# Optimization experiments

Measured on AMD Instinct MI355X. Metric: run time of the kernel, lower is better.

## Reference

```python
import jax, jax.numpy as jnp
import numpy as np

B, NN, F, H = 8, 1024, 256, 8
D = F // H
SCALE = D ** -0.5


def setup_inputs() -> dict:
    key = jax.random.key(0)
    ks = jax.random.split(key, 12)
    s = 0.02
    inp = {
        'ndata': jax.random.normal(ks[0], (B, NN, F), jnp.float32),
        'N': NN,
        'attn_bias': jax.random.normal(ks[1], (B, NN, NN, H), jnp.float32),
        'attn_mask': jax.random.randint(ks[2], (B, NN, NN), 0, 2).astype(bool),
        'Wq': jax.random.normal(ks[3], (F, F), jnp.float32) * s,
        'bq': jnp.zeros((F,), jnp.float32),
        'Wk': jax.random.normal(ks[4], (F, F), jnp.float32) * s,
        'bk': jnp.zeros((F,), jnp.float32),
        'Wv': jax.random.normal(ks[5], (F, F), jnp.float32) * s,
        'bv': jnp.zeros((F,), jnp.float32),
        'Wo': jax.random.normal(ks[6], (F, F), jnp.float32) * s,
        'bo': jnp.zeros((F,), jnp.float32),
    }
    return inp


def reference(ndata, N, attn_bias, attn_mask, Wq, bq, Wk, bk, Wv, bv, Wo, bo):
    b, n, f = ndata.shape
    # QKV projections (torch nn.Linear: x @ W.T + b), split heads
    q = (ndata @ Wq.T + bq).reshape(b, n, H, D) * SCALE
    k = (ndata @ Wk.T + bk).reshape(b, n, H, D)
    v = (ndata @ Wv.T + bv).reshape(b, n, H, D)
    # scores: (b, q, k, h) matching torch layout after its transposes
    scores = jnp.einsum('bqhd,bkhd->bqkh', q, k)
    scores = scores + attn_bias  # additive bias
    # original code force-unmasks column 0 so every row has a valid entry
    mask = attn_mask.at[:, :, 0].set(False)
    scores = jnp.where(mask[..., None], -jnp.inf, scores)
    attn = jax.nn.softmax(scores, axis=2)  # softmax over keys
    out = jnp.einsum('bqkh,bkhd->bqhd', attn, v).reshape(b, n, f)
    return out @ Wo.T + bo
```

## Files before the change

### kernel.cpp

```cpp
#include <hip/hip_runtime.h>
#include <hip/hip_bf16.h>

typedef __attribute__((ext_vector_type(8))) short short8;
typedef __attribute__((ext_vector_type(4))) float f32x4;

#define MFMA16(a,b,c) __builtin_amdgcn_mfma_f32_16x16x32_bf16((a),(b),(c),0,0,0)

static __device__ __forceinline__ unsigned int f2bf(float f){
    unsigned int u = __float_as_uint(f);
    u += 0x7FFFu + ((u >> 16) & 1u);
    return u >> 16;
}

static __device__ __forceinline__ short8 pack8(float4 a, float4 b){
    short8 r;
    r[0]=(short)f2bf(a.x); r[1]=(short)f2bf(a.y);
    r[2]=(short)f2bf(a.z); r[3]=(short)f2bf(a.w);
    r[4]=(short)f2bf(b.x); r[5]=(short)f2bf(b.y);
    r[6]=(short)f2bf(b.z); r[7]=(short)f2bf(b.w);
    return r;
}

__global__ void detect_mask_k(const int* __restrict__ m, int* __restrict__ flag){
    __shared__ int any_hi;
    if (threadIdx.x == 0) any_hi = 0;
    __syncthreads();
    int acc = 0;
    #pragma unroll
    for (int it = 0; it < 16; ++it)
        acc |= m[it*256 + threadIdx.x];
    if (acc & 0xFFFFFF00) atomicOr(&any_hi, 1);
    __syncthreads();
    if (threadIdx.x == 0) *flag = any_hi;
}

__global__ __launch_bounds__(256) void mask_prep_k(
    const unsigned int* __restrict__ m, const int* __restrict__ flag,
    unsigned int* __restrict__ bmout)
{
    const int tid  = threadIdx.x;
    const int lane = tid & 63;
    const unsigned int gbase = blockIdx.x*256u + tid;
    if (*flag == 0){
        for (int it = 0; it < 32; ++it){
            unsigned int idx = it*262144u + gbase;
            unsigned int v = m[idx];
            unsigned long long bal = __ballot(v != 0u);
            if (lane == 0)
                *(unsigned long long*)(bmout + (idx >> 5)) = bal;
        }
    } else {
        for (int it = 0; it < 8; ++it){
            unsigned int idx = it*262144u + gbase;
            unsigned int v = m[idx];
            unsigned int nib = (v | (v>>7) | (v>>14) | (v>>21)) & 0xFu;
            unsigned int x = nib << ((lane & 7)*4);
            x |= (unsigned int)__shfl_xor((int)x, 1);
            x |= (unsigned int)__shfl_xor((int)x, 2);
            x |= (unsigned int)__shfl_xor((int)x, 4);
            if ((lane & 7) == 0)
                bmout[idx >> 3] = x;
        }
    }
}

__global__ __launch_bounds__(256) void qkv_proj_k(
    const float* __restrict__ nd,
    const float* __restrict__ Wqp, const float* __restrict__ bqp,
    const float* __restrict__ Wkp, const float* __restrict__ bkp,
    const float* __restrict__ Wvp, const float* __restrict__ bvp,
    unsigned short* __restrict__ qout, unsigned short* __restrict__ kout,
    unsigned short* __restrict__ vtout)
{
    __shared__ __align__(16) unsigned short xl[64*264];
    const int tid  = threadIdx.x;
    const int bi   = blockIdx.x;
    const int kind = bi >> 7;
    const int R0   = (bi & 127) * 64;
    const int b    = R0 >> 10;
    const int n0   = R0 & 1023;

    #pragma unroll
    for (int it = 0; it < 16; ++it){
        int f4 = it*256 + tid;
        int r = f4 >> 6, c4 = f4 & 63;
        float4 v = *(const float4*)(nd + (size_t)(R0+r)*256 + c4*4);
        unsigned int lo = f2bf(v.x) | (f2bf(v.y) << 16);
        unsigned int hi = f2bf(v.z) | (f2bf(v.w) << 16);
        *(uint2*)&xl[r*264 + c4*4] = make_uint2(lo, hi);
    }
    __syncthreads();

    const int lane = tid & 63;
    const int w  = tid >> 6;
    const int ln = lane & 15;
    const int g  = lane >> 4;
    const int ow = w * 64;

    f32x4 acc[4][4];
    #pragma unroll
    for (int a=0;a<4;++a){
        #pragma unroll
        for (int c=0;c<4;++c) acc[a][c] = (f32x4){0.f,0.f,0.f,0.f};
    }

    if (kind < 2){
        const float* W  = kind ? Wkp : Wqp;
        const float* bb = kind ? bkp : bqp;
        unsigned short* op = kind ? kout : qout;
        const float scl = kind ? 1.0f : 0.17677669529663687f;
        for (int kk = 0; kk < 8; ++kk){
            short8 wf[4], xf[4];
            #pragma unroll
            for (int ot=0; ot<4; ++ot){
                const float* wp = W + (size_t)(ow + ot*16 + ln)*256 + kk*32 + g*8;
                wf[ot] = pack8(*(const float4*)wp, *(const float4*)(wp+4));
            }
            #pragma unroll
            for (int nt=0; nt<4; ++nt)
                xf[nt] = *(const short8*)&xl[(nt*16+ln)*264 + kk*32 + g*8];
            #pragma unroll
            for (int ot=0; ot<4; ++ot){
                #pragma unroll
                for (int nt=0; nt<4; ++nt)
                    acc[ot][nt] = MFMA16(wf[ot], xf[nt], acc[ot][nt]);
            }
        }
        #pragma unroll
        for (int ot=0; ot<4; ++ot){
            int o0 = ow + ot*16 + g*4;
            int h = o0 >> 5, d0 = o0 & 31;
            float4 b4 = *(const float4*)(bb + o0);
            #pragma unroll
            for (int nt=0; nt<4; ++nt){
                int n = n0 + nt*16 + ln;
                unsigned int lo = f2bf((acc[ot][nt][0]+b4.x)*scl) | (f2bf((acc[ot][nt][1]+b4.y)*scl)<<16);
                unsigned int hi = f2bf((acc[ot][nt][2]+b4.z)*scl) | (f2bf((acc[ot][nt][3]+b4.w)*scl)<<16);
                *(uint2*)(op + ((size_t)(b*8+h)*1024 + n)*32 + d0) = make_uint2(lo,hi);
            }
        }
    } else {
        for (int kk = 0; kk < 8; ++kk){
            short8 wf[4], xf[4];
            #pragma unroll
            for (int ot=0; ot<4; ++ot){
                const float* wp = Wvp + (size_t)(ow + ot*16 + ln)*256 + kk*32 + g*8;
                wf[ot] = pack8(*(const float4*)wp, *(const float4*)(wp+4));
            }
            #pragma unroll
            for (int nt=0; nt<4; ++nt)
                xf[nt] = *(const short8*)&xl[(nt*16+ln)*264 + kk*32 + g*8];
            #pragma unroll
            for (int nt=0; nt<4; ++nt){
                #pragma unroll
                for (int ot=0; ot<4; ++ot)
                    acc[nt][ot] = MFMA16(xf[nt], wf[ot], acc[nt][ot]);
            }
        }
        #pragma unroll
        for (int nt=0; nt<4; ++nt){
            int nb = n0 + nt*16 + g*4;
            #pragma unroll
            for (int ot=0; ot<4; ++ot){
                int o = ow + ot*16 + ln;
                int h = o >> 5, d = o & 31;
                float bvv = bvp[o];
                unsigned int lo = f2bf(acc[nt][ot][0]+bvv) | (f2bf(acc[nt][ot][1]+bvv)<<16);
                unsigned int hi = f2bf(acc[nt][ot][2]+bvv) | (f2bf(acc[nt][ot][3]+bvv)<<16);
                *(uint2*)(vtout + ((size_t)(b*8+h)*32 + d)*1024 + nb) = make_uint2(lo,hi);
            }
        }
    }
}

__global__ __launch_bounds__(512, 4) void attn_k(
    const unsigned short* __restrict__ qbuf, const unsigned short* __restrict__ kbuf,
    const unsigned short* __restrict__ vtbuf, const float* __restrict__ bias,
    const unsigned int* __restrict__ bm, unsigned short* __restrict__ ab)
{
    __shared__ float bs[4096];
    const int tid  = threadIdx.x;
    const int bi   = blockIdx.x;
    const int b    = bi >> 6;
    const int q0   = (bi & 63) * 16;
    const int lane = tid & 63;
    const int w    = tid >> 6;
    const int ln   = lane & 15;
    const int g    = lane >> 4;

    const short8 qf = *(const short8*)(qbuf + ((size_t)(b*8+w)*1024 + q0 + ln)*32 + g*8);

    const int h2s  = lane & 1;
    const int keys = lane >> 1;
    const int ts   = keys >> 4;
    const int rs   = keys & 3;
    const int gs   = (keys >> 2) & 3;
    const int base0 = (128*ts + 32*rs + 16*h2s + gs) * 16;
    const int xrs   = (8*ts + 2*rs + h2s) & 15;
    const int qxa   = (2*w)     ^ xrs;
    const int qxb   = (2*w + 1) ^ xrs;

    const float* bp0 = bias + ((size_t)(b*1024 + q0 + 2*w)*1024)*8 + lane*4;
    const unsigned short* kp = kbuf  + ((size_t)(b*8+w)*1024 + ln)*32 + g*8;
    const unsigned short* vp = vtbuf + ((size_t)(b*8+w)*32   + ln)*1024 + g*8;
    const unsigned int*  bmp = bm + (size_t)(b*1024 + q0 + ln)*32;

    f32x4 acc0 = (f32x4){0.f,0.f,0.f,0.f};
    f32x4 acc1 = (f32x4){0.f,0.f,0.f,0.f};
    float m_ = -1e30f, l_ = 0.f;
    const f32x4 z4 = {0.f,0.f,0.f,0.f};

    float4 ba  = *(const float4*)(bp0);
    float4 bb2 = *(const float4*)(bp0 + 8192);
    short8 kn0 = *(const short8*)(kp);
    short8 kn1 = *(const short8*)(kp + 512);
    short8 vn0 = *(const short8*)(vp);
    short8 vn1 = *(const short8*)(vp + 16*1024);
    unsigned int bmn = bmp[0] & ~1u;

    for (int c = 0; c < 32; ++c){
        bs[base0       + qxa] = ba.x;  bs[base0 +  64 + qxa] = ba.y;
        bs[base0 + 128 + qxa] = ba.z;  bs[base0 + 192 + qxa] = ba.w;
        bs[base0       + qxb] = bb2.x; bs[base0 +  64 + qxb] = bb2.y;
        bs[base0 + 128 + qxb] = bb2.z; bs[base0 + 192 + qxb] = bb2.w;

        short8 kc0 = kn0, kc1 = kn1, vc0 = vn0, vc1 = vn1;
        unsigned int bmc = bmn;

        if (c < 31){
            int c1 = c + 1;
            ba  = *(const float4*)(bp0 + c1*256);
            bb2 = *(const float4*)(bp0 + c1*256 + 8192);
            kn0 = *(const short8*)(kp + c1*1024);
            kn1 = *(const short8*)(kp + c1*1024 + 512);
            vn0 = *(const short8*)(vp + c1*32);
            vn1 = *(const short8*)(vp + c1*32 + 16*1024);
            bmn = bmp[c1];
        }
        __syncthreads();

        f32x4 s0 = MFMA16(kc0, qf, z4);
        f32x4 s1 = MFMA16(kc1, qf, z4);

        float pv[8];
        float mx = -1e30f;
        #pragma unroll
        for (int t=0; t<2; ++t){
            #pragma unroll
            for (int r=0; r<4; ++r){
                int keyl = t*16 + g*4 + r;
                int bidx = (t*128 + r*32 + w*4 + g)*16 + (ln ^ ((t*8 + r*2 + (w>>2)) & 15));
                float sv = (t ? s1[r] : s0[r]) + bs[bidx];
                sv = ((bmc >> keyl) & 1u) ? -1e30f : sv;
                pv[t*4+r] = sv;
                mx = fmaxf(mx, sv);
            }
        }
        mx = fmaxf(mx, __shfl_xor(mx, 16));
        mx = fmaxf(mx, __shfl_xor(mx, 32));
        float mn = fmaxf(m_, mx);
        float alpha = __expf(m_ - mn);
        m_ = mn;
        float ps = 0.f;
        #pragma unroll
        for (int i=0;i<8;++i){ pv[i] = __expf(pv[i]-mn); ps += pv[i]; }
        ps += __shfl_xor(ps, 16);
        ps += __shfl_xor(ps, 32);
        l_ = l_*alpha + ps;
        #pragma unroll
        for (int r=0;r<4;++r){ acc0[r]*=alpha; acc1[r]*=alpha; }

        unsigned int A01 = f2bf(pv[0]) | (f2bf(pv[1])<<16);
        unsigned int A23 = f2bf(pv[2]) | (f2bf(pv[3])<<16);
        unsigned int B01 = f2bf(pv[4]) | (f2bf(pv[5])<<16);
        unsigned int B23 = f2bf(pv[6]) | (f2bf(pv[7])<<16);
        int s0l = (2*(g&1))*16 + ln;
        int s1l = s0l + 16;
        unsigned int a01  = (unsigned int)__shfl((int)A01, s0l);
        unsigned int a23  = (unsigned int)__shfl((int)A23, s0l);
        unsigned int b01  = (unsigned int)__shfl((int)B01, s0l);
        unsigned int b23  = (unsigned int)__shfl((int)B23, s0l);
        unsigned int a01b = (unsigned int)__shfl((int)A01, s1l);
        unsigned int a23b = (unsigned int)__shfl((int)A23, s1l);
        unsigned int b01b = (unsigned int)__shfl((int)B01, s1l);
        unsigned int b23b = (unsigned int)__shfl((int)B23, s1l);
        bool hi = (g >= 2);
        int4 pw = make_int4((int)(hi ? b01  : a01 ), (int)(hi ? b23  : a23 ),
                            (int)(hi ? b01b : a01b), (int)(hi ? b23b : a23b));
        short8 pf = *(short8*)&pw;

        acc0 = MFMA16(vc0, pf, acc0);
        acc1 = MFMA16(vc1, pf, acc1);
        __syncthreads();
    }

    float inv = 1.0f / l_;
    {
        int n = q0 + ln;
        unsigned int lo0 = f2bf(acc0[0]*inv) | (f2bf(acc0[1]*inv)<<16);
        unsigned int hi0 = f2bf(acc0[2]*inv) | (f2bf(acc0[3]*inv)<<16);
        *(uint2*)(ab + ((size_t)(b*1024 + n))*256 + w*32 + g*4) = make_uint2(lo0,hi0);
        unsigned int lo1 = f2bf(acc1[0]*inv) | (f2bf(acc1[1]*inv)<<16);
        unsigned int hi1 = f2bf(acc1[2]*inv) | (f2bf(acc1[3]*inv)<<16);
        *(uint2*)(ab + ((size_t)(b*1024 + n))*256 + w*32 + 16 + g*4) = make_uint2(lo1,hi1);
    }
}

__global__ __launch_bounds__(256) void oproj_k(
    const unsigned short* __restrict__ ab, const float* __restrict__ Wop,
    const float* __restrict__ bop, float* __restrict__ out)
{
    __shared__ __align__(16) unsigned short al[32*264];
    const int tid = threadIdx.x;
    const int R0 = blockIdx.x * 32;
    #pragma unroll
    for (int it=0; it<4; ++it){
        int f8 = it*256 + tid;
        int r = f8 >> 5, c8 = f8 & 31;
        *(short8*)&al[r*264 + c8*8] = *(const short8*)(ab + (size_t)(R0+r)*256 + c8*8);
    }
    __syncthreads();
    const int lane = tid & 63;
    const int w = tid >> 6, ln = lane & 15, g = lane >> 4;
    const int ow = w*64;
    f32x4 acc[4][2];
    #pragma unroll
    for (int a=0;a<4;++a){ acc[a][0]=(f32x4){0.f,0.f,0.f,0.f}; acc[a][1]=(f32x4){0.f,0.f,0.f,0.f}; }
    for (int kk=0;kk<8;++kk){
        short8 wf[4], xf[2];
        #pragma unroll
        for (int ot=0;ot<4;++ot){
            const float* wp = Wop + (size_t)(ow+ot*16+ln)*256 + kk*32 + g*8;
            wf[ot] = pack8(*(const float4*)wp, *(const float4*)(wp+4));
        }
        #pragma unroll
        for (int nt=0;nt<2;++nt)
            xf[nt] = *(const short8*)&al[(nt*16+ln)*264 + kk*32 + g*8];
        #pragma unroll
        for (int ot=0;ot<4;++ot){
            #pragma unroll
            for (int nt=0;nt<2;++nt)
                acc[ot][nt] = MFMA16(wf[ot], xf[nt], acc[ot][nt]);
        }
    }
    #pragma unroll
    for (int ot=0;ot<4;++ot){
        int o0 = ow + ot*16 + g*4;
        float4 b4 = *(const float4*)(bop + o0);
        #pragma unroll
        for (int nt=0;nt<2;++nt){
            int n = R0 + nt*16 + ln;
            float4 res;
            res.x = acc[ot][nt][0] + b4.x;
            res.y = acc[ot][nt][1] + b4.y;
            res.z = acc[ot][nt][2] + b4.z;
            res.w = acc[ot][nt][3] + b4.w;
            *(float4*)(out + (size_t)n*256 + o0) = res;
        }
    }
}

extern "C" void kernel_launch(void* const* d_in, const int* in_sizes, int n_in,
                              void* d_out, int out_size, void* d_ws, size_t ws_size,
                              hipStream_t stream)
{
    (void)in_sizes; (void)n_in; (void)out_size; (void)ws_size;
    const float* nd   = (const float*)d_in[0];
    const float* bias = (const float*)d_in[2];
    const int* mask   = (const int*)d_in[3];
    const float* Wq = (const float*)d_in[4];
    const float* bq = (const float*)d_in[5];
    const float* Wk = (const float*)d_in[6];
    const float* bk = (const float*)d_in[7];
    const float* Wv = (const float*)d_in[8];
    const float* bv = (const float*)d_in[9];
    const float* Wo = (const float*)d_in[10];
    const float* bo = (const float*)d_in[11];
    float* out = (float*)d_out;

    const size_t ELEMS = (size_t)8*8*1024*32;
    unsigned short* qb  = (unsigned short*)d_ws;
    unsigned short* kb  = qb  + ELEMS;
    unsigned short* vtb = kb  + ELEMS;
    unsigned short* ab  = vtb + ELEMS;
    unsigned int* bmw   = (unsigned int*)(ab + ELEMS);
    int* mflag          = (int*)(bmw + 262144);

    detect_mask_k<<<1, 256, 0, stream>>>(mask, mflag);
    mask_prep_k<<<1024, 256, 0, stream>>>((const unsigned int*)mask, mflag, bmw);
    qkv_proj_k<<<384, 256, 0, stream>>>(nd, Wq, bq, Wk, bk, Wv, bv, qb, kb, vtb);
    attn_k<<<512, 512, 0, stream>>>(qb, kb, vtb, bias, bmw, ab);
    oproj_k<<<256, 256, 0, stream>>>(ab, Wo, bo, out);
}
```

Baseline: 146.9 us.

## Drop online softmax max tracking, split heads across blocks, fuse mask detection

Removes the running-max and rescaling from the attention softmax. It exponentiates biased scores directly and sums them per lane, reducing across lanes once at the end. Keys are permuted so P fragments line up with the MFMA layout without cross-lane shuffles, and each block now handles 4 heads instead of 8, doubling the grid. The loop is unrolled 2x with double-buffered K/V loads, and the separate mask-detection kernel is folded into mask_prep, with the format check now made per block. Skipping the max subtraction risks overflow when scores or biases are large.

New measurement: 170.3 us. 1.16x slower.

```diff
diff --git a/kernel.cpp b/kernel.cpp
--- a/kernel.cpp
+++ b/kernel.cpp
@@ -21,27 +21,26 @@
     return r;
 }
 
-__global__ void detect_mask_k(const int* __restrict__ m, int* __restrict__ flag){
+__global__ __launch_bounds__(256) void mask_prep_k(
+    const unsigned int* __restrict__ m, unsigned int* __restrict__ bmout)
+{
     __shared__ int any_hi;
-    if (threadIdx.x == 0) any_hi = 0;
-    __syncthreads();
-    int acc = 0;
-    #pragma unroll
-    for (int it = 0; it < 16; ++it)
-        acc |= m[it*256 + threadIdx.x];
-    if (acc & 0xFFFFFF00) atomicOr(&any_hi, 1);
-    __syncthreads();
-    if (threadIdx.x == 0) *flag = any_hi;
-}
-
-__global__ __launch_bounds__(256) void mask_prep_k(
-    const unsigned int* __restrict__ m, const int* __restrict__ flag,
-    unsigned int* __restrict__ bmout)
-{
     const int tid  = threadIdx.x;
     const int lane = tid & 63;
     const unsigned int gbase = blockIdx.x*256u + tid;
-    if (*flag == 0){
+    if (tid == 0) any_hi = 0;
+
+    unsigned int wv[8]; unsigned int acc = 0;
+    #pragma unroll
+    for (int it = 0; it < 8; ++it){
+        wv[it] = m[it*262144u + gbase];
+        acc |= wv[it];
+    }
+    __syncthreads();
+    if (acc & 0xFFFFFF00u) atomicOr(&any_hi, 1);
+    __syncthreads();
+
+    if (any_hi == 0){
         for (int it = 0; it < 32; ++it){
             unsigned int idx = it*262144u + gbase;
             unsigned int v = m[idx];
@@ -50,9 +49,10 @@
                 *(unsigned long long*)(bmout + (idx >> 5)) = bal;
         }
     } else {
+        #pragma unroll
         for (int it = 0; it < 8; ++it){
             unsigned int idx = it*262144u + gbase;
-            unsigned int v = m[idx];
+            unsigned int v = wv[it];
             unsigned int nib = (v | (v>>7) | (v>>14) | (v>>21)) & 0xFu;
             unsigned int x = nib << ((lane & 7)*4);
             x |= (unsigned int)__shfl_xor((int)x, 1);
@@ -173,137 +173,125 @@
     }
 }
 
-__global__ __launch_bounds__(512, 4) void attn_k(
+__global__ __launch_bounds__(256, 4) void attn_k(
     const unsigned short* __restrict__ qbuf, const unsigned short* __restrict__ kbuf,
     const unsigned short* __restrict__ vtbuf, const float* __restrict__ bias,
     const unsigned int* __restrict__ bm, unsigned short* __restrict__ ab)
 {
-    __shared__ float bs[4096];
+    __shared__ float bs[2048];
     const int tid  = threadIdx.x;
     const int bi   = blockIdx.x;
-    const int b    = bi >> 6;
-    const int q0   = (bi & 63) * 16;
+    const int hh   = bi & 1;
+    const int qt   = (bi >> 1) & 63;
+    const int b    = bi >> 7;
+    const int q0   = qt * 16;
     const int lane = tid & 63;
     const int w    = tid >> 6;
     const int ln   = lane & 15;
     const int g    = lane >> 4;
-
-    const short8 qf = *(const short8*)(qbuf + ((size_t)(b*8+w)*1024 + q0 + ln)*32 + g*8);
-
-    const int h2s  = lane & 1;
-    const int keys = lane >> 1;
-    const int ts   = keys >> 4;
-    const int rs   = keys & 3;
-    const int gs   = (keys >> 2) & 3;
-    const int base0 = (128*ts + 32*rs + 16*h2s + gs) * 16;
-    const int xrs   = (8*ts + 2*rs + h2s) & 15;
-    const int qxa   = (2*w)     ^ xrs;
-    const int qxb   = (2*w + 1) ^ xrs;
-
-    const float* bp0 = bias + ((size_t)(b*1024 + q0 + 2*w)*1024)*8 + lane*4;
-    const unsigned short* kp = kbuf  + ((size_t)(b*8+w)*1024 + ln)*32 + g*8;
-    const unsigned short* vp = vtbuf + ((size_t)(b*8+w)*32   + ln)*1024 + g*8;
-    const unsigned int*  bmp = bm + (size_t)(b*1024 + q0 + ln)*32;
+    const int h    = hh*4 + w;
+
+    const short8 qf = *(const short8*)(qbuf + ((size_t)(b*8+h)*1024 + q0 + ln)*32 + g*8);
+
+    const int kperm = ((ln >> 2) << 3) + (ln & 3);
+    const unsigned short* kp = kbuf  + ((size_t)(b*8+h)*1024 + kperm)*32 + g*8;
+    const unsigned short* vp = vtbuf + ((size_t)(b*8+h)*32 + ln)*1024 + g*8;
+    const unsigned int* bmp  = bm + (size_t)(b*1024 + q0 + ln)*32;
+
+    const int qt0 = tid >> 5;
+    const int kk0 = tid & 31;
+    const float* bgp0 = bias + ((size_t)(b*1024 + q0 + qt0)*1024 + kk0)*8 + hh*4;
+    const float* bgp1 = bgp0 + 65536;
+    const int kx  = kk0 ^ qt0;
+    const int w0i = qt0*32 + kx;
+    const int w1i = w0i + 256;
+
+    const int base_rg = w*512 + ln*32 + g*8;
+    const int lnx = ln & 7;
 
     f32x4 acc0 = (f32x4){0.f,0.f,0.f,0.f};
     f32x4 acc1 = (f32x4){0.f,0.f,0.f,0.f};
-    float m_ = -1e30f, l_ = 0.f;
+    float lsum = 0.f;
     const f32x4 z4 = {0.f,0.f,0.f,0.f};
 
-    float4 ba  = *(const float4*)(bp0);
-    float4 bb2 = *(const float4*)(bp0 + 8192);
-    short8 kn0 = *(const short8*)(kp);
-    short8 kn1 = *(const short8*)(kp + 512);
-    short8 vn0 = *(const short8*)(vp);
-    short8 vn1 = *(const short8*)(vp + 16*1024);
-    unsigned int bmn = bmp[0] & ~1u;
-
-    for (int c = 0; c < 32; ++c){
-        bs[base0       + qxa] = ba.x;  bs[base0 +  64 + qxa] = ba.y;
-        bs[base0 + 128 + qxa] = ba.z;  bs[base0 + 192 + qxa] = ba.w;
-        bs[base0       + qxb] = bb2.x; bs[base0 +  64 + qxb] = bb2.y;
-        bs[base0 + 128 + qxb] = bb2.z; bs[base0 + 192 + qxb] = bb2.w;
-
-        short8 kc0 = kn0, kc1 = kn1, vc0 = vn0, vc1 = vn1;
-        unsigned int bmc = bmn;
-
-        if (c < 31){
-            int c1 = c + 1;
-            ba  = *(const float4*)(bp0 + c1*256);
-            bb2 = *(const float4*)(bp0 + c1*256 + 8192);
-            kn0 = *(const short8*)(kp + c1*1024);
-            kn1 = *(const short8*)(kp + c1*1024 + 512);
-            vn0 = *(const short8*)(vp + c1*32);
-            vn1 = *(const short8*)(vp + c1*32 + 16*1024);
-            bmn = bmp[c1];
-        }
+    float4 br0, br1;
+    short8 kA0, kA1, vA0, vA1, kB0, kB1, vB0, vB1;
+    unsigned int bmA, bmB;
+
+#define LOAD_BIAS(cc) do { int c_=(cc); \
+    br0 = *(const float4*)(bgp0 + c_*256); \
+    br1 = *(const float4*)(bgp1 + c_*256); } while(0)
+
+#define STAGE() do { \
+    bs[w0i       ] = br0.x; bs[w0i +  512] = br0.y; \
+    bs[w0i + 1024] = br0.z; bs[w0i + 1536] = br0.w; \
+    bs[w1i       ] = br1.x; bs[w1i +  512] = br1.y; \
+    bs[w1i + 1024] = br1.z; bs[w1i + 1536] = br1.w; } while(0)
+
+#define LOAD_KVM(S, cc) do { int c_=(cc); \
+    k##S##0 = *(const short8*)(kp + c_*1024); \
+    k##S##1 = *(const short8*)(kp + c_*1024 + 128); \
+    v##S##0 = *(const short8*)(vp + c_*32); \
+    v##S##1 = *(const short8*)(vp + c_*32 + 16*1024); \
+    bm##S   = bmp[c_]; } while(0)
+
+#define COMPUTE(S) do { \
+    unsigned int mb_ = bm##S >> (g*8); \
+    f32x4 s0 = MFMA16(k##S##0, qf, z4); \
+    f32x4 s1 = MFMA16(k##S##1, qf, z4); \
+    float e0 = __expf(((mb_>>0)&1u) ? -1e30f : s0[0] + bs[base_rg + (0^lnx)]); \
+    float e1 = __expf(((mb_>>1)&1u) ? -1e30f : s0[1] + bs[base_rg + (1^lnx)]); \
+    float e2 = __expf(((mb_>>2)&1u) ? -1e30f : s0[2] + bs[base_rg + (2^lnx)]); \
+    float e3 = __expf(((mb_>>3)&1u) ? -1e30f : s0[3] + bs[base_rg + (3^lnx)]); \
+    float e4 = __expf(((mb_>>4)&1u) ? -1e30f : s1[0] + bs[base_rg + (4^lnx)]); \
+    float e5 = __expf(((mb_>>5)&1u) ? -1e30f : s1[1] + bs[base_rg + (5^lnx)]); \
+    float e6 = __expf(((mb_>>6)&1u) ? -1e30f : s1[2] + bs[base_rg + (6^lnx)]); \
+    float e7 = __expf(((mb_>>7)&1u) ? -1e30f : s1[3] + bs[base_rg + (7^lnx)]); \
+    lsum += ((e0+e1)+(e2+e3)) + ((e4+e5)+(e6+e7)); \
+    int4 pw_ = make_int4( \
+        (int)(f2bf(e0) | (f2bf(e1)<<16)), (int)(f2bf(e2) | (f2bf(e3)<<16)), \
+        (int)(f2bf(e4) | (f2bf(e5)<<16)), (int)(f2bf(e6) | (f2bf(e7)<<16))); \
+    short8 pf_ = *(short8*)&pw_; \
+    acc0 = MFMA16(v##S##0, pf_, acc0); \
+    acc1 = MFMA16(v##S##1, pf_, acc1); } while(0)
+
+    LOAD_BIAS(0);
+    LOAD_KVM(A, 0);
+    bmA &= ~1u;
+
+    #pragma unroll 1
+    for (int c = 0; c < 32; c += 2){
+        STAGE();
+        LOAD_BIAS(c + 1);
         __syncthreads();
-
-        f32x4 s0 = MFMA16(kc0, qf, z4);
-        f32x4 s1 = MFMA16(kc1, qf, z4);
-
-        float pv[8];
-        float mx = -1e30f;
-        #pragma unroll
-        for (int t=0; t<2; ++t){
-            #pragma unroll
-            for (int r=0; r<4; ++r){
-                int keyl = t*16 + g*4 + r;
-                int bidx = (t*128 + r*32 + w*4 + g)*16 + (ln ^ ((t*8 + r*2 + (w>>2)) & 15));
-                float sv = (t ? s1[r] : s0[r]) + bs[bidx];
-                sv = ((bmc >> keyl) & 1u) ? -1e30f : sv;
-                pv[t*4+r] = sv;
-                mx = fmaxf(mx, sv);
-            }
-        }
-        mx = fmaxf(mx, __shfl_xor(mx, 16));
-        mx = fmaxf(mx, __shfl_xor(mx, 32));
-        float mn = fmaxf(m_, mx);
-        float alpha = __expf(m_ - mn);
-        m_ = mn;
-        float ps = 0.f;
-        #pragma unroll
-        for (int i=0;i<8;++i){ pv[i] = __expf(pv[i]-mn); ps += pv[i]; }
-        ps += __shfl_xor(ps, 16);
-        ps += __shfl_xor(ps, 32);
-        l_ = l_*alpha + ps;
-        #pragma unroll
-        for (int r=0;r<4;++r){ acc0[r]*=alpha; acc1[r]*=alpha; }
-
-        unsigned int A01 = f2bf(pv[0]) | (f2bf(pv[1])<<16);
-        unsigned int A23 = f2bf(pv[2]) | (f2bf(pv[3])<<16);
-        unsigned int B01 = f2bf(pv[4]) | (f2bf(pv[5])<<16);
-        unsigned int B23 = f2bf(pv[6]) | (f2bf(pv[7])<<16);
-        int s0l = (2*(g&1))*16 + ln;
-        int s1l = s0l + 16;
-        unsigned int a01  = (unsigned int)__shfl((int)A01, s0l);
-        unsigned int a23  = (unsigned int)__shfl((int)A23, s0l);
-        unsigned int b01  = (unsigned int)__shfl((int)B01, s0l);
-        unsigned int b23  = (unsigned int)__shfl((int)B23, s0l);
-        unsigned int a01b = (unsigned int)__shfl((int)A01, s1l);
-        unsigned int a23b = (unsigned int)__shfl((int)A23, s1l);
-        unsigned int b01b = (unsigned int)__shfl((int)B01, s1l);
-        unsigned int b23b = (unsigned int)__shfl((int)B23, s1l);
-        bool hi = (g >= 2);
-        int4 pw = make_int4((int)(hi ? b01  : a01 ), (int)(hi ? b23  : a23 ),
-                            (int)(hi ? b01b : a01b), (int)(hi ? b23b : a23b));
-        short8 pf = *(short8*)&pw;
-
-        acc0 = MFMA16(vc0, pf, acc0);
-        acc1 = MFMA16(vc1, pf, acc1);
+        LOAD_KVM(B, c + 1);
+        COMPUTE(A);
         __syncthreads();
-    }
-
-    float inv = 1.0f / l_;
+        STAGE();
+        if (c + 2 < 32) LOAD_BIAS(c + 2);
+        __syncthreads();
+        if (c + 2 < 32) LOAD_KVM(A, c + 2);
+        COMPUTE(B);
+        __syncthreads();
+    }
+
+    float ps = lsum;
+    ps += __shfl_xor(ps, 16);
+    ps += __shfl_xor(ps, 32);
+    float inv = 1.0f / ps;
     {
-        int n = q0 + ln;
+        size_t orow = ((size_t)(b*1024 + q0 + ln))*256 + h*32;
         unsigned int lo0 = f2bf(acc0[0]*inv) | (f2bf(acc0[1]*inv)<<16);
         unsigned int hi0 = f2bf(acc0[2]*inv) | (f2bf(acc0[3]*inv)<<16);
-        *(uint2*)(ab + ((size_t)(b*1024 + n))*256 + w*32 + g*4) = make_uint2(lo0,hi0);
+        *(uint2*)(ab + orow + g*4) = make_uint2(lo0,hi0);
         unsigned int lo1 = f2bf(acc1[0]*inv) | (f2bf(acc1[1]*inv)<<16);
         unsigned int hi1 = f2bf(acc1[2]*inv) | (f2bf(acc1[3]*inv)<<16);
-        *(uint2*)(ab + ((size_t)(b*1024 + n))*256 + w*32 + 16 + g*4) = make_uint2(lo1,hi1);
-    }
+        *(uint2*)(ab + orow + 16 + g*4) = make_uint2(lo1,hi1);
+    }
+#undef LOAD_BIAS
+#undef STAGE
+#undef LOAD_KVM
+#undef COMPUTE
 }
 
 __global__ __launch_bounds__(256) void oproj_k(
@@ -384,11 +372,9 @@
     unsigned short* vtb = kb  + ELEMS;
     unsigned short* ab  = vtb + ELEMS;
     unsigned int* bmw   = (unsigned int*)(ab + ELEMS);
-    int* mflag          = (int*)(bmw + 262144);
-
-    detect_mask_k<<<1, 256, 0, stream>>>(mask, mflag);
-    mask_prep_k<<<1024, 256, 0, stream>>>((const unsigned int*)mask, mflag, bmw);
+
+    mask_prep_k<<<1024, 256, 0, stream>>>((const unsigned int*)mask, bmw);
     qkv_proj_k<<<384, 256, 0, stream>>>(nd, Wq, bq, Wk, bk, Wv, bv, qb, kb, vtb);
-    attn_k<<<512, 512, 0, stream>>>(qb, kb, vtb, bias, bmw, ab);
+    attn_k<<<1024, 256, 0, stream>>>(qb, kb, vtb, bias, bmw, ab);
     oproj_k<<<256, 256, 0, stream>>>(ab, Wo, bo, out);
 }
```
